# Performance work log

Measured on AMD Instinct MI355X. Metric: run time of the kernel, lower is better.

Reference implementation:

```python
import jax, jax.numpy as jnp
import numpy as np

N_NODES = 50000
N_EDGES = 800000
NUM_GRAPHS = 256
EPS = 1e-5


def _gcn_conv(x, edge_index, W, b):
    # PyG GCNConv: add self-loops, sym-normalize, aggregate, then add bias.
    n = x.shape[0]
    xw = x @ W  # [N, out]
    loops = jnp.arange(n)
    row = jnp.concatenate([edge_index[0], loops])  # source
    col = jnp.concatenate([edge_index[1], loops])  # target
    deg = jax.ops.segment_sum(jnp.ones_like(col, dtype=xw.dtype), col, num_segments=n)
    dinv = jnp.where(deg > 0, jax.lax.rsqrt(deg), 0.0)
    norm = dinv[row] * dinv[col]  # [E+N]
    msg = norm[:, None] * xw[row]  # gather + scale
    out = jax.ops.segment_sum(msg, col, num_segments=n)  # scatter-add
    return out + b


def _bn(x, g, b, m, v):
    # inference-mode batch norm
    return (x - m) * jax.lax.rsqrt(v + EPS) * g + b


def reference(x, edge_index, batch, gcn_W0, gcn_b0, bn_g0, bn_b0, bn_m0, bn_v0,
              gcn_W1, gcn_b1, bn_g1, bn_b1, bn_m1, bn_v1,
              hW1, hb1, hg1, hbb1, hm1, hv1,
              hW2, hb2, hg2, hbb2, hm2, hv2,
              hW3, hb3, hW4, hb4):
    # GCN block 0
    h = _gcn_conv(x, edge_index, gcn_W0, gcn_b0)
    h = jax.nn.relu(_bn(h, bn_g0, bn_b0, bn_m0, bn_v0))  # dropout = identity (eval)
    # GCN block 1
    h = _gcn_conv(h, edge_index, gcn_W1, gcn_b1)
    h = jax.nn.relu(_bn(h, bn_g1, bn_b1, bn_m1, bn_v1))
    # global mean pool over graphs
    sums = jax.ops.segment_sum(h, batch, num_segments=NUM_GRAPHS)
    cnts = jax.ops.segment_sum(jnp.ones_like(batch, dtype=h.dtype), batch, num_segments=NUM_GRAPHS)
    pooled = sums / jnp.maximum(cnts, 1.0)[:, None]  # [G, 64]
    # MLP head (eval: dropout identity)
    z = jax.nn.relu(_bn(pooled @ hW1 + hb1, hg1, hbb1, hm1, hv1))
    z = jax.nn.relu(_bn(z @ hW2 + hb2, hg2, hbb2, hm2, hv2))
    z = jax.nn.relu(z @ hW3 + hb3)
    out = (z @ hW4 + hb4).reshape(-1)  # [G]
    return out


def setup_inputs() -> dict:
    key = jax.random.key(0)
    ks = jax.random.split(key, 12)
    d = 64
    inp = {
        'x': jax.random.normal(ks[0], (N_NODES, d), dtype=jnp.float32),
        'edge_index': jax.random.randint(ks[1], (2, N_EDGES), 0, N_NODES, dtype=jnp.int64),
        'batch': jnp.sort(jax.random.randint(ks[2], (N_NODES,), 0, NUM_GRAPHS, dtype=jnp.int64)),
        'gcn_W0': jax.random.normal(ks[3], (d, d), dtype=jnp.float32) * 0.1,
        'gcn_b0': jnp.zeros((d,), jnp.float32),
        'bn_g0': jnp.ones((d,), jnp.float32), 'bn_b0': jnp.zeros((d,), jnp.float32),
        'bn_m0': jnp.zeros((d,), jnp.float32), 'bn_v0': jnp.ones((d,), jnp.float32),
        'gcn_W1': jax.random.normal(ks[4], (d, d), dtype=jnp.float32) * 0.1,
        'gcn_b1': jnp.zeros((d,), jnp.float32),
        'bn_g1': jnp.ones((d,), jnp.float32), 'bn_b1': jnp.zeros((d,), jnp.float32),
        'bn_m1': jnp.zeros((d,), jnp.float32), 'bn_v1': jnp.ones((d,), jnp.float32),
        'hW1': jax.random.normal(ks[5], (d, 256), dtype=jnp.float32) * 0.1,
        'hb1': jnp.zeros((256,), jnp.float32),
        'hg1': jnp.ones((256,), jnp.float32), 'hbb1': jnp.zeros((256,), jnp.float32),
        'hm1': jnp.zeros((256,), jnp.float32), 'hv1': jnp.ones((256,), jnp.float32),
        'hW2': jax.random.normal(ks[6], (256, 128), dtype=jnp.float32) * 0.1,
        'hb2': jnp.zeros((128,), jnp.float32),
        'hg2': jnp.ones((128,), jnp.float32), 'hbb2': jnp.zeros((128,), jnp.float32),
        'hm2': jnp.zeros((128,), jnp.float32), 'hv2': jnp.ones((128,), jnp.float32),
        'hW3': jax.random.normal(ks[7], (128, 64), dtype=jnp.float32) * 0.1,
        'hb3': jnp.zeros((64,), jnp.float32),
        'hW4': jax.random.normal(ks[8], (64, 1), dtype=jnp.float32) * 0.1,
        'hb4': jnp.zeros((1,), jnp.float32),
    }
    return inp
```

## Files before the change

kernel.cpp:

```cpp
#include <hip/hip_runtime.h>
#include <hip/hip_bf16.h>
#include <hip/hip_fp16.h>

#define N_NODES 50000
#define N_EDGES 800000
#define NUM_GRAPHS 256
#define D 64
#define EPS 1e-5f
#define N_PART 8
#define PART_SIZE (N_NODES / N_PART)
#define SCAT_CHUNKS 512
#define SCAT_GRID (SCAT_CHUNKS * N_PART)
#define GEMM_BLOCKS ((N_NODES + 63) / 64)
#define WP 72

typedef _Float16 half8_t __attribute__((ext_vector_type(8)));
typedef float f32x4 __attribute__((ext_vector_type(4)));

__device__ __forceinline__ void acc16(const uint4& v, float w, float4& A, float4& B) {
    const __half2* hp = (const __half2*)&v;
    float2 q0 = __half22float2(hp[0]), q1 = __half22float2(hp[1]);
    float2 q2 = __half22float2(hp[2]), q3 = __half22float2(hp[3]);
    A.x += w * q0.x; A.y += w * q0.y; A.z += w * q1.x; A.w += w * q1.y;
    B.x += w * q2.x; B.y += w * q2.y; B.z += w * q3.x; B.w += w * q3.y;
}

__global__ __launch_bounds__(256) void build_gemm_kernel(
        const int* __restrict__ ei, int* __restrict__ cnt,
        unsigned short* __restrict__ ssrc, int cap,
        const float* __restrict__ X, const float* __restrict__ W,
        __half* __restrict__ Yh) {
    __shared__ _Float16 Xs[64 * WP];
    __shared__ _Float16 Wt[64 * WP];
    if (blockIdx.x < SCAT_GRID) {
        int p     = blockIdx.x & (N_PART - 1);
        int chunk = blockIdx.x >> 3;
        const int per = (((N_EDGES + SCAT_CHUNKS - 1) / SCAT_CHUNKS) + 3) & ~3;
        int lo = chunk * per;
        int hi = lo + per; if (hi > N_EDGES) hi = N_EDGES;
        for (int e4 = lo + (int)threadIdx.x * 4; e4 < hi; e4 += 1024) {
            int4 c4 = *(const int4*)&ei[N_EDGES + e4];
            const int* cc = (const int*)&c4;
#pragma unroll
            for (int k = 0; k < 4; k++) {
                int e = e4 + k;
                if (e < hi) {
                    int c = cc[k];
                    if (c / PART_SIZE == p) {
                        int r = ei[e];
                        int pos = atomicAdd(&cnt[c], 1);
                        if (pos < cap) ssrc[(size_t)c * cap + pos] = (unsigned short)r;
                    }
                }
            }
        }
        return;
    }
    int tid  = threadIdx.x;
    int base = (blockIdx.x - SCAT_GRID) * 64;
    for (int i = tid; i < 4096; i += 256) {
        int k = i >> 6, n = i & 63;
        Wt[n * WP + k] = (_Float16)W[i];
    }
    for (int i = tid; i < 1024; i += 256) {
        int r = i >> 4, c4 = (i & 15) * 4;
        float4 xv = (base + r < N_NODES)
            ? ((const float4*)X)[(size_t)(base + r) * 16 + (i & 15)]
            : make_float4(0.f, 0.f, 0.f, 0.f);
        _Float16* dst = &Xs[r * WP + c4];
        dst[0] = (_Float16)xv.x; dst[1] = (_Float16)xv.y;
        dst[2] = (_Float16)xv.z; dst[3] = (_Float16)xv.w;
    }
    __syncthreads();
    int wave  = tid >> 6;
    int lane  = tid & 63;
    int m     = lane & 15;
    int q     = lane >> 4;
    int row16 = wave * 16;
    half8_t a0 = *(const half8_t*)&Xs[(row16 + m) * WP + q * 8];
    half8_t a1 = *(const half8_t*)&Xs[(row16 + m) * WP + 32 + q * 8];
    f32x4 acc[4];
#pragma unroll
    for (int ct = 0; ct < 4; ct++) {
        half8_t b0 = *(const half8_t*)&Wt[(ct * 16 + m) * WP + q * 8];
        half8_t b1 = *(const half8_t*)&Wt[(ct * 16 + m) * WP + 32 + q * 8];
        f32x4 c = {0.f, 0.f, 0.f, 0.f};
        c = __builtin_amdgcn_mfma_f32_16x16x32_f16(a0, b0, c, 0, 0, 0);
        c = __builtin_amdgcn_mfma_f32_16x16x32_f16(a1, b1, c, 0, 0, 0);
        acc[ct] = c;
    }
#pragma unroll
    for (int ct = 0; ct < 4; ct++) {
#pragma unroll
        for (int reg = 0; reg < 4; reg++) {
            int row = base + row16 + q * 4 + reg;
            if (row < N_NODES)
                Yh[(size_t)row * 64 + ct * 16 + m] = (__half)acc[ct][reg];
        }
    }
}

__global__ __launch_bounds__(256) void scale_kernel(__half* __restrict__ xwh,
                                                    const int* __restrict__ cnt,
                                                    int N) {
    int i = blockIdx.x * 256 + threadIdx.x;
    if (i >= N * 8) return;
    int row = i >> 3;
    float w = rsqrtf((float)cnt[row] + 1.0f);
    uint4 v = ((const uint4*)xwh)[i];
    __half2* hp = (__half2*)&v;
#pragma unroll
    for (int j = 0; j < 4; j++) {
        float2 q = __half22float2(hp[j]);
        hp[j] = __floats2half2_rn(q.x * w, q.y * w);
    }
    ((uint4*)xwh)[i] = v;
}

__global__ __launch_bounds__(256) void agg_bn_kernel(
        const __half* __restrict__ xwh, const int* __restrict__ cnt,
        const unsigned short* __restrict__ ssrc, int cap,
        const float* __restrict__ b, const float* __restrict__ g,
        const float* __restrict__ bb, const float* __restrict__ m,
        const float* __restrict__ var,
        float* __restrict__ out, int N) {
    int wave = (blockIdx.x * blockDim.x + threadIdx.x) >> 6;
    int lane = threadIdx.x & 63;
    if (wave >= N) return;
    int c   = wave;
    int sub = lane >> 3;
    int f2  = lane & 7;
    const uint4* xw8 = (const uint4*)xwh;
    int n = cnt[c];
    if (n > cap) n = cap;
    float dc = rsqrtf((float)n + 1.0f);
    size_t sbase = (size_t)c * cap;
    int idx = (lane < cap) ? (int)ssrc[sbase + lane] : 0;
    uint4 vself = make_uint4(0u, 0u, 0u, 0u);
    if (sub == 0) vself = xw8[(size_t)c * 8 + f2];
    int t = (n + 7) >> 3;
    float4 accA = make_float4(0.f, 0.f, 0.f, 0.f);
    float4 accB = accA;
    uint4 vc = make_uint4(0u, 0u, 0u, 0u);
    float wc = 0.0f;
    if (t > 0) {
        int r0 = __shfl(idx, sub, 64);
        wc = (sub < n) ? 1.0f : 0.0f;
        if (sub >= n) r0 = c;
        vc = xw8[(size_t)r0 * 8 + f2];
    }
    for (int k = 1; k < t; k++) {
        int s  = k * 8 + sub;
        int r1 = __shfl(idx, s, 64);
        float wn = (s < n) ? 1.0f : 0.0f;
        if (s >= n) r1 = c;
        uint4 vn = xw8[(size_t)r1 * 8 + f2];
        acc16(vc, wc, accA, accB);
        vc = vn; wc = wn;
    }
    if (t > 0) acc16(vc, wc, accA, accB);
    if (sub == 0) acc16(vself, 1.0f, accA, accB);
#pragma unroll
    for (int off = 8; off < 64; off <<= 1) {
        accA.x += __shfl_xor(accA.x, off, 64); accA.y += __shfl_xor(accA.y, off, 64);
        accA.z += __shfl_xor(accA.z, off, 64); accA.w += __shfl_xor(accA.w, off, 64);
        accB.x += __shfl_xor(accB.x, off, 64); accB.y += __shfl_xor(accB.y, off, 64);
        accB.z += __shfl_xor(accB.z, off, 64); accB.w += __shfl_xor(accB.w, off, 64);
    }
    if (sub < 2) {
        int i4 = 2 * f2 + sub;
        float4 acc = sub ? accB : accA;
        float4 b4  = ((const float4*)b)[i4];
        float4 m4  = ((const float4*)m)[i4];
        float4 v4_ = ((const float4*)var)[i4];
        float4 g4  = ((const float4*)g)[i4];
        float4 bb4 = ((const float4*)bb)[i4];
        float4 h;
        h.x = (acc.x * dc + b4.x - m4.x) * (1.0f / sqrtf(v4_.x + EPS)) * g4.x + bb4.x;
        h.y = (acc.y * dc + b4.y - m4.y) * (1.0f / sqrtf(v4_.y + EPS)) * g4.y + bb4.y;
        h.z = (acc.z * dc + b4.z - m4.z) * (1.0f / sqrtf(v4_.z + EPS)) * g4.z + bb4.z;
        h.w = (acc.w * dc + b4.w - m4.w) * (1.0f / sqrtf(v4_.w + EPS)) * g4.w + bb4.w;
        h.x = h.x > 0.f ? h.x : 0.f;
        h.y = h.y > 0.f ? h.y : 0.f;
        h.z = h.z > 0.f ? h.z : 0.f;
        h.w = h.w > 0.f ? h.w : 0.f;
        ((float4*)out)[(size_t)c * 16 + i4] = h;
    }
}

__global__ __launch_bounds__(256) void gemm64_kernel(const float* __restrict__ X,
                                                     const float* __restrict__ W,
                                                     const int* __restrict__ cnt,
                                                     __half* __restrict__ Yh, int N) {
    __shared__ _Float16 Xs[64 * WP];
    __shared__ _Float16 Wt[64 * WP];
    int tid  = threadIdx.x;
    int base = blockIdx.x * 64;
    for (int i = tid; i < 4096; i += 256) {
        int k = i >> 6, n = i & 63;
        Wt[n * WP + k] = (_Float16)W[i];
    }
    for (int i = tid; i < 1024; i += 256) {
        int r = i >> 4, c4 = (i & 15) * 4;
        float4 xv = (base + r < N)
            ? ((const float4*)X)[(size_t)(base + r) * 16 + (i & 15)]
            : make_float4(0.f, 0.f, 0.f, 0.f);
        _Float16* dst = &Xs[r * WP + c4];
        dst[0] = (_Float16)xv.x; dst[1] = (_Float16)xv.y;
        dst[2] = (_Float16)xv.z; dst[3] = (_Float16)xv.w;
    }
    __syncthreads();
    int wave  = tid >> 6;
    int lane  = tid & 63;
    int m     = lane & 15;
    int q     = lane >> 4;
    int row16 = wave * 16;
    half8_t a0 = *(const half8_t*)&Xs[(row16 + m) * WP + q * 8];
    half8_t a1 = *(const half8_t*)&Xs[(row16 + m) * WP + 32 + q * 8];
    f32x4 acc[4];
#pragma unroll
    for (int ct = 0; ct < 4; ct++) {
        half8_t b0 = *(const half8_t*)&Wt[(ct * 16 + m) * WP + q * 8];
        half8_t b1 = *(const half8_t*)&Wt[(ct * 16 + m) * WP + 32 + q * 8];
        f32x4 c = {0.f, 0.f, 0.f, 0.f};
        c = __builtin_amdgcn_mfma_f32_16x16x32_f16(a0, b0, c, 0, 0, 0);
        c = __builtin_amdgcn_mfma_f32_16x16x32_f16(a1, b1, c, 0, 0, 0);
        acc[ct] = c;
    }
    int   rows[4];
    float ws[4];
#pragma unroll
    for (int reg = 0; reg < 4; reg++) {
        rows[reg] = base + row16 + q * 4 + reg;
        ws[reg] = (rows[reg] < N) ? rsqrtf((float)cnt[rows[reg]] + 1.0f) : 0.0f;
    }
#pragma unroll
    for (int ct = 0; ct < 4; ct++) {
#pragma unroll
        for (int reg = 0; reg < 4; reg++) {
            if (rows[reg] < N)
                Yh[(size_t)rows[reg] * 64 + ct * 16 + m] =
                    (__half)(ws[reg] * acc[ct][reg]);
        }
    }
}

__global__ __launch_bounds__(256) void pool_head_kernel(
        const float* __restrict__ h, const int* __restrict__ batch,
        const float* __restrict__ hW1, const float* __restrict__ hb1,
        const float* __restrict__ hg1, const float* __restrict__ hbb1,
        const float* __restrict__ hm1, const float* __restrict__ hv1,
        const float* __restrict__ hW2, const float* __restrict__ hb2,
        const float* __restrict__ hg2, const float* __restrict__ hbb2,
        const float* __restrict__ hm2, const float* __restrict__ hv2,
        const float* __restrict__ hW3, const float* __restrict__ hb3,
        const float* __restrict__ hW4, const float* __restrict__ hb4,
        float* __restrict__ out) {
    __shared__ int se[2];
    __shared__ float red[256];
    __shared__ float pooled[64];
    __shared__ float z1[256];
    __shared__ float z2[128];
    __shared__ float z3[64];
    int g = blockIdx.x;
    int t = threadIdx.x;
    if (t < 2) {
        int target = g + t;
        int lo = 0, hi = N_NODES;
        while (lo < hi) {
            int mid = (lo + hi) >> 1;
            if (batch[mid] < target) lo = mid + 1; else hi = mid;
        }
        se[t] = lo;
    }
    __syncthreads();
    int start = se[0], end = se[1];
    {
        int f = t & 63, rg = t >> 6;
        float part = 0.0f;
        for (int r = start + rg; r < end; r += 4) part += h[(size_t)r * 64 + f];
        red[t] = part;
        __syncthreads();
        if (t < 64) {
            float s = red[t] + red[t + 64] + red[t + 128] + red[t + 192];
            float cnt = (float)(end - start);
            cnt = cnt > 1.0f ? cnt : 1.0f;
            pooled[t] = s / cnt;
        }
    }
    __syncthreads();
    {
        float acc = hb1[t];
#pragma unroll
        for (int k = 0; k < 64; k++) acc += pooled[k] * hW1[k * 256 + t];
        acc = (acc - hm1[t]) * (1.0f / sqrtf(hv1[t] + EPS)) * hg1[t] + hbb1[t];
        z1[t] = acc > 0.0f ? acc : 0.0f;
    }
    __syncthreads();
    if (t < 128) {
        float acc = hb2[t];
#pragma unroll 8
        for (int k = 0; k < 256; k++) acc += z1[k] * hW2[k * 128 + t];
        acc = (acc - hm2[t]) * (1.0f / sqrtf(hv2[t] + EPS)) * hg2[t] + hbb2[t];
        z2[t] = acc > 0.0f ? acc : 0.0f;
    }
    __syncthreads();
    if (t < 64) {
        float acc = hb3[t];
#pragma unroll 8
        for (int k = 0; k < 128; k++) acc += z2[k] * hW3[k * 64 + t];
        z3[t] = acc > 0.0f ? acc : 0.0f;
    }
    __syncthreads();
    if (t < 64) {
        float v = z3[t] * hW4[t];
        for (int off = 32; off > 0; off >>= 1) v += __shfl_down(v, off, 64);
        if (t == 0) out[g] = v + hb4[0];
    }
}

extern "C" void kernel_launch(void* const* d_in, const int* in_sizes, int n_in,
                              void* d_out, int out_size, void* d_ws, size_t ws_size,
                              hipStream_t stream) {
    const float* x     = (const float*)d_in[0];
    const int*   ei    = (const int*)d_in[1];
    const int*   batch = (const int*)d_in[2];
    const float* W0 = (const float*)d_in[3];
    const float* b0 = (const float*)d_in[4];
    const float* g0 = (const float*)d_in[5];
    const float* bb0 = (const float*)d_in[6];
    const float* m0 = (const float*)d_in[7];
    const float* v0 = (const float*)d_in[8];
    const float* W1 = (const float*)d_in[9];
    const float* b1 = (const float*)d_in[10];
    const float* g1 = (const float*)d_in[11];
    const float* bb1 = (const float*)d_in[12];
    const float* m1 = (const float*)d_in[13];
    const float* v1 = (const float*)d_in[14];
    const float* hW1 = (const float*)d_in[15];
    const float* hb1 = (const float*)d_in[16];
    const float* hg1 = (const float*)d_in[17];
    const float* hbb1 = (const float*)d_in[18];
    const float* hm1 = (const float*)d_in[19];
    const float* hv1 = (const float*)d_in[20];
    const float* hW2 = (const float*)d_in[21];
    const float* hb2 = (const float*)d_in[22];
    const float* hg2 = (const float*)d_in[23];
    const float* hbb2 = (const float*)d_in[24];
    const float* hm2 = (const float*)d_in[25];
    const float* hv2 = (const float*)d_in[26];
    const float* hW3 = (const float*)d_in[27];
    const float* hb3 = (const float*)d_in[28];
    const float* hW4 = (const float*)d_in[29];
    const float* hb4 = (const float*)d_in[30];
    float* out = (float*)d_out;

    __half* xwhA = (__half*)d_ws;
    __half* xwhB = xwhA + (size_t)N_NODES * D;
    float*  bufB = (float*)(xwhB + (size_t)N_NODES * D);
    int*    cnt  = (int*)(bufB + (size_t)N_NODES * D);
    unsigned short* ssrc = (unsigned short*)(cnt + N_NODES);

    size_t used = (size_t)2 * N_NODES * D * 2 + (size_t)N_NODES * D * 4
                + (size_t)N_NODES * 4;
    int cap = 64;
    if (ws_size >= used) {
        size_t avail = (ws_size - used) / ((size_t)N_NODES * 2);
        if (avail < (size_t)cap) cap = (int)avail & ~7;
    } else {
        cap = 0;
    }

    const int NT = 256;
    hipMemsetAsync(cnt, 0, (size_t)N_NODES * 4, stream);

    build_gemm_kernel<<<SCAT_GRID + GEMM_BLOCKS, NT, 0, stream>>>(
        ei, cnt, ssrc, cap, x, W0, xwhA);

    scale_kernel<<<(N_NODES * 8 + NT - 1) / NT, NT, 0, stream>>>(xwhA, cnt, N_NODES);

    agg_bn_kernel<<<(N_NODES * 64) / NT, NT, 0, stream>>>(
        xwhA, cnt, ssrc, cap, b0, g0, bb0, m0, v0, bufB, N_NODES);

    gemm64_kernel<<<GEMM_BLOCKS, NT, 0, stream>>>(bufB, W1, cnt, xwhB, N_NODES);

    agg_bn_kernel<<<(N_NODES * 64) / NT, NT, 0, stream>>>(
        xwhB, cnt, ssrc, cap, b1, g1, bb1, m1, v1, bufB, N_NODES);

    pool_head_kernel<<<NUM_GRAPHS, NT, 0, stream>>>(bufB, batch,
        hW1, hb1, hg1, hbb1, hm1, hv1,
        hW2, hb2, hg2, hbb2, hm2, hv2,
        hW3, hb3, hW4, hb4, out);
}
```

Before: 261.7 us.

## Fold source degree scaling into aggregation, fp16 intermediate, reorder build blocks

Removes the separate scale kernel and the per-row degree scaling in the second GEMM. The aggregation kernel now loads cnt[src] for each neighbor and applies rsqrt weighting in flight, using a two-deep prefetch pipeline. The first layer's BN output is stored as fp16 so the second GEMM reads half-precision rows directly. GEMM blocks are placed before scatter blocks in the combined build kernel, and X is read with nontemporal loads. This trades one kernel launch and a full read/write pass for an extra gather of cnt per edge, and slightly lower precision of the intermediate activations.

```diff
diff --git a/kernel.cpp b/kernel.cpp
--- a/kernel.cpp
+++ b/kernel.cpp
@@ -15,6 +15,7 @@
 #define WP 72
 
 typedef _Float16 half8_t __attribute__((ext_vector_type(8)));
+typedef _Float16 half4_t __attribute__((ext_vector_type(4)));
 typedef float f32x4 __attribute__((ext_vector_type(4)));
 
 __device__ __forceinline__ void acc16(const uint4& v, float w, float4& A, float4& B) {
@@ -32,9 +33,10 @@
         __half* __restrict__ Yh) {
     __shared__ _Float16 Xs[64 * WP];
     __shared__ _Float16 Wt[64 * WP];
-    if (blockIdx.x < SCAT_GRID) {
+    if (blockIdx.x >= GEMM_BLOCKS) {
+        int scat  = blockIdx.x - GEMM_BLOCKS;
         int p     = blockIdx.x & (N_PART - 1);
-        int chunk = blockIdx.x >> 3;
+        int chunk = scat >> 3;
         const int per = (((N_EDGES + SCAT_CHUNKS - 1) / SCAT_CHUNKS) + 3) & ~3;
         int lo = chunk * per;
         int hi = lo + per; if (hi > N_EDGES) hi = N_EDGES;
@@ -57,16 +59,20 @@
         return;
     }
     int tid  = threadIdx.x;
-    int base = (blockIdx.x - SCAT_GRID) * 64;
+    int base = blockIdx.x * 64;
     for (int i = tid; i < 4096; i += 256) {
         int k = i >> 6, n = i & 63;
         Wt[n * WP + k] = (_Float16)W[i];
     }
     for (int i = tid; i < 1024; i += 256) {
         int r = i >> 4, c4 = (i & 15) * 4;
-        float4 xv = (base + r < N_NODES)
-            ? ((const float4*)X)[(size_t)(base + r) * 16 + (i & 15)]
-            : make_float4(0.f, 0.f, 0.f, 0.f);
+        f32x4 xv;
+        if (base + r < N_NODES) {
+            xv = __builtin_nontemporal_load(
+                     &((const f32x4*)X)[(size_t)(base + r) * 16 + (i & 15)]);
+        } else {
+            xv = (f32x4){0.f, 0.f, 0.f, 0.f};
+        }
         _Float16* dst = &Xs[r * WP + c4];
         dst[0] = (_Float16)xv.x; dst[1] = (_Float16)xv.y;
         dst[2] = (_Float16)xv.z; dst[3] = (_Float16)xv.w;
@@ -100,30 +106,14 @@
     }
 }
 
-__global__ __launch_bounds__(256) void scale_kernel(__half* __restrict__ xwh,
-                                                    const int* __restrict__ cnt,
-                                                    int N) {
-    int i = blockIdx.x * 256 + threadIdx.x;
-    if (i >= N * 8) return;
-    int row = i >> 3;
-    float w = rsqrtf((float)cnt[row] + 1.0f);
-    uint4 v = ((const uint4*)xwh)[i];
-    __half2* hp = (__half2*)&v;
-#pragma unroll
-    for (int j = 0; j < 4; j++) {
-        float2 q = __half22float2(hp[j]);
-        hp[j] = __floats2half2_rn(q.x * w, q.y * w);
-    }
-    ((uint4*)xwh)[i] = v;
-}
-
+template<bool OUTF16>
 __global__ __launch_bounds__(256) void agg_bn_kernel(
         const __half* __restrict__ xwh, const int* __restrict__ cnt,
         const unsigned short* __restrict__ ssrc, int cap,
         const float* __restrict__ b, const float* __restrict__ g,
         const float* __restrict__ bb, const float* __restrict__ m,
         const float* __restrict__ var,
-        float* __restrict__ out, int N) {
+        void* __restrict__ out, int N) {
     int wave = (blockIdx.x * blockDim.x + threadIdx.x) >> 6;
     int lane = threadIdx.x & 63;
     if (wave >= N) return;
@@ -141,25 +131,28 @@
     int t = (n + 7) >> 3;
     float4 accA = make_float4(0.f, 0.f, 0.f, 0.f);
     float4 accB = accA;
-    uint4 vc = make_uint4(0u, 0u, 0u, 0u);
-    float wc = 0.0f;
-    if (t > 0) {
-        int r0 = __shfl(idx, sub, 64);
-        wc = (sub < n) ? 1.0f : 0.0f;
-        if (sub >= n) r0 = c;
-        vc = xw8[(size_t)r0 * 8 + f2];
-    }
-    for (int k = 1; k < t; k++) {
-        int s  = k * 8 + sub;
-        int r1 = __shfl(idx, s, 64);
-        float wn = (s < n) ? 1.0f : 0.0f;
-        if (s >= n) r1 = c;
-        uint4 vn = xw8[(size_t)r1 * 8 + f2];
-        acc16(vc, wc, accA, accB);
-        vc = vn; wc = wn;
-    }
-    if (t > 0) acc16(vc, wc, accA, accB);
-    if (sub == 0) acc16(vself, 1.0f, accA, accB);
+
+    uint4 v0 = make_uint4(0u,0u,0u,0u), v1 = v0;
+    int   cv0 = -1, cv1 = -1;
+    auto issue = [&](int k, uint4& v, int& cv) {
+        int s = k * 8 + sub;
+        int sc = (s < n) ? s : 0;
+        int r  = __shfl(idx, sc, 64);
+        if (s >= n) r = c;
+        cv = (s < n) ? cnt[r] : -1;
+        v  = xw8[(size_t)r * 8 + f2];
+    };
+    auto consume = [&](const uint4& v, int cv) {
+        if (cv >= 0) acc16(v, rsqrtf((float)cv + 1.0f), accA, accB);
+    };
+    if (t > 0) issue(0, v0, cv0);
+    if (t > 1) issue(1, v1, cv1);
+    for (int k = 0; k < t; k++) {
+        consume(v0, cv0);
+        v0 = v1; cv0 = cv1;
+        if (k + 2 < t) issue(k + 2, v1, cv1); else cv1 = -1;
+    }
+    if (sub == 0) acc16(vself, dc, accA, accB);
 #pragma unroll
     for (int off = 8; off < 64; off <<= 1) {
         accA.x += __shfl_xor(accA.x, off, 64); accA.y += __shfl_xor(accA.y, off, 64);
@@ -184,14 +177,18 @@
         h.y = h.y > 0.f ? h.y : 0.f;
         h.z = h.z > 0.f ? h.z : 0.f;
         h.w = h.w > 0.f ? h.w : 0.f;
-        ((float4*)out)[(size_t)c * 16 + i4] = h;
-    }
-}
-
-__global__ __launch_bounds__(256) void gemm64_kernel(const float* __restrict__ X,
-                                                     const float* __restrict__ W,
-                                                     const int* __restrict__ cnt,
-                                                     __half* __restrict__ Yh, int N) {
+        if (OUTF16) {
+            half4_t hv = {(_Float16)h.x, (_Float16)h.y, (_Float16)h.z, (_Float16)h.w};
+            *(half4_t*)((__half*)out + (size_t)c * 64 + i4 * 4) = hv;
+        } else {
+            ((float4*)out)[(size_t)c * 16 + i4] = h;
+        }
+    }
+}
+
+__global__ __launch_bounds__(256) void gemm64h_kernel(const __half* __restrict__ Xh,
+                                                      const float* __restrict__ W,
+                                                      __half* __restrict__ Yh, int N) {
     __shared__ _Float16 Xs[64 * WP];
     __shared__ _Float16 Wt[64 * WP];
     int tid  = threadIdx.x;
@@ -200,14 +197,12 @@
         int k = i >> 6, n = i & 63;
         Wt[n * WP + k] = (_Float16)W[i];
     }
-    for (int i = tid; i < 1024; i += 256) {
-        int r = i >> 4, c4 = (i & 15) * 4;
-        float4 xv = (base + r < N)
-            ? ((const float4*)X)[(size_t)(base + r) * 16 + (i & 15)]
-            : make_float4(0.f, 0.f, 0.f, 0.f);
-        _Float16* dst = &Xs[r * WP + c4];
-        dst[0] = (_Float16)xv.x; dst[1] = (_Float16)xv.y;
-        dst[2] = (_Float16)xv.z; dst[3] = (_Float16)xv.w;
+    for (int i = tid; i < 512; i += 256) {
+        int r = i >> 3, c8 = (i & 7) * 8;
+        uint4 v = (base + r < N)
+            ? ((const uint4*)Xh)[(size_t)(base + r) * 8 + (i & 7)]
+            : make_uint4(0u, 0u, 0u, 0u);
+        *(uint4*)&Xs[r * WP + c8] = v;
     }
     __syncthreads();
     int wave  = tid >> 6;
@@ -227,20 +222,13 @@
         c = __builtin_amdgcn_mfma_f32_16x16x32_f16(a1, b1, c, 0, 0, 0);
         acc[ct] = c;
     }
-    int   rows[4];
-    float ws[4];
-#pragma unroll
-    for (int reg = 0; reg < 4; reg++) {
-        rows[reg] = base + row16 + q * 4 + reg;
-        ws[reg] = (rows[reg] < N) ? rsqrtf((float)cnt[rows[reg]] + 1.0f) : 0.0f;
-    }
 #pragma unroll
     for (int ct = 0; ct < 4; ct++) {
 #pragma unroll
         for (int reg = 0; reg < 4; reg++) {
-            if (rows[reg] < N)
-                Yh[(size_t)rows[reg] * 64 + ct * 16 + m] =
-                    (__half)(ws[reg] * acc[ct][reg]);
+            int row = base + row16 + q * 4 + reg;
+            if (row < N)
+                Yh[(size_t)row * 64 + ct * 16 + m] = (__half)acc[ct][reg];
         }
     }
 }
@@ -377,15 +365,13 @@
     build_gemm_kernel<<<SCAT_GRID + GEMM_BLOCKS, NT, 0, stream>>>(
         ei, cnt, ssrc, cap, x, W0, xwhA);
 
-    scale_kernel<<<(N_NODES * 8 + NT - 1) / NT, NT, 0, stream>>>(xwhA, cnt, N_NODES);
-
-    agg_bn_kernel<<<(N_NODES * 64) / NT, NT, 0, stream>>>(
-        xwhA, cnt, ssrc, cap, b0, g0, bb0, m0, v0, bufB, N_NODES);
-
-    gemm64_kernel<<<GEMM_BLOCKS, NT, 0, stream>>>(bufB, W1, cnt, xwhB, N_NODES);
-
-    agg_bn_kernel<<<(N_NODES * 64) / NT, NT, 0, stream>>>(
-        xwhB, cnt, ssrc, cap, b1, g1, bb1, m1, v1, bufB, N_NODES);
+    agg_bn_kernel<true><<<(N_NODES * 64) / NT, NT, 0, stream>>>(
+        xwhA, cnt, ssrc, cap, b0, g0, bb0, m0, v0, xwhB, N_NODES);
+
+    gemm64h_kernel<<<GEMM_BLOCKS, NT, 0, stream>>>(xwhB, W1, xwhA, N_NODES);
+
+    agg_bn_kernel<false><<<(N_NODES * 64) / NT, NT, 0, stream>>>(
+        xwhA, cnt, ssrc, cap, b1, g1, bb1, m1, v1, bufB, N_NODES);
 
     pool_head_kernel<<<NUM_GRAPHS, NT, 0, stream>>>(bufB, batch,
         hW1, hb1, hg1, hbb1, hm1, hv1,
```

Result: no change. 258.2 us (-1.3%).
